# Kernel optimization log

Measured on AMD Instinct MI355X. Metric: run time of the kernel, lower is better.

## Reference

```python
import jax, jax.numpy as jnp
import numpy as np

EPS = 1e-8
SMOOTH = 9.0   # lambda_softmax
STEPS = 3      # iteration_step
SLOPE = 0.1    # LeakyReLU slope used by clipped_l2norm


def l2norm(x, axis=-1):
    # matches torch l2norm: x / (sqrt(sum x^2) + eps)
    return x / (jnp.sqrt(jnp.sum(x * x, axis=axis, keepdims=True)) + EPS)


def cos_sim(a, b, axis=-1):
    num = jnp.sum(a * b, axis=axis)
    den = jnp.linalg.norm(a, axis=axis) * jnp.linalg.norm(b, axis=axis)
    return num / jnp.maximum(den, EPS)


def duplicate_mask(cap):
    # same_word logic: cap_k identical to cap_c (off-diagonal). Computed via
    # pairwise squared distances (one GEMM) instead of O(B^2 L d) direct compare.
    B = cap.shape[0]
    flat = cap.reshape(B, -1)
    sq = jnp.sum(flat * flat, axis=1)
    d2 = sq[:, None] + sq[None, :] - 2.0 * (flat @ flat.T)
    return (d2 <= 1e-6) & (~jnp.eye(B, dtype=bool))


def gated(q, a, Wl, bl, Wg, bg):
    cat = jnp.concatenate([q, a], axis=-1)            # (..., 2d)
    lin = jnp.tanh(cat @ Wl.T + bl)
    gate = jax.nn.sigmoid(cat @ Wg.T + bg)
    return q * gate + lin * (1.0 - gate)


def imram_forward(img, cap, W_lt2i, b_lt2i, W_gt2i, b_gt2i,
                  W_li2t, b_li2t, W_gi2t, b_gi2t):
    B, R, D = img.shape
    L = cap.shape[1]
    dup = duplicate_mask(cap)                         # symmetric
    total = jnp.zeros((B, B), img.dtype)              # [caption, image] (training=True transpose)

    # ---- text-to-image: query = caption words, context = image regions ----
    cap_e = jnp.broadcast_to(cap[:, None], (B, B, L, D))   # (cap c, img i, L, D)
    q = cap_e
    for _ in range(STEPS):
        attn = jnp.einsum('ird,cild->cirl', img, q)          # (c,i,R,L)
        attn = l2norm(jax.nn.leaky_relu(attn, SLOPE), axis=-1)   # clipped_l2norm over queryL
        attn = jax.nn.softmax(SMOOTH * attn, axis=2)             # softmax over source regions r
        wc = jnp.einsum('cirl,ird->cild', attn, img)             # weightedContext (c,i,L,D)
        sim = jnp.mean(cos_sim(cap_e, wc, axis=-1), axis=-1)    # (c,i)
        total = total + jnp.where(dup, -1.0, sim)
        q = l2norm(gated(q, wc, W_lt2i, b_lt2i, W_gt2i, b_gt2i), axis=-1)

    # ---- image-to-text: query = image regions, context = caption words ----
    img_e = jnp.broadcast_to(img[None], (B, B, R, D))
    q = img_e
    for _ in range(STEPS):
        attn = jnp.einsum('cld,cird->cilr', cap, q)          # (c,i,L,R)
        attn = l2norm(jax.nn.leaky_relu(attn, SLOPE), axis=-1)   # over queryL (= R)
        attn = jax.nn.softmax(SMOOTH * attn, axis=2)             # over source words l
        wc = jnp.einsum('cilr,cld->cird', attn, cap)             # (c,i,R,D)
        sim = jnp.mean(cos_sim(img_e, wc, axis=-1), axis=-1)
        total = total + jnp.where(dup, -1.0, sim)
        q = l2norm(gated(q, wc, W_li2t, b_li2t, W_gi2t, b_gi2t), axis=-1)

    return total


def setup_inputs() -> dict:
    key = jax.random.key(0)
    ks = jax.random.split(key, 8)
    B, R, L, D = 32, 36, 40, 1024
    img_emb = jax.random.normal(ks[0], (B, R, D), dtype=jnp.float32)
    cap_emb = jax.random.normal(ks[1], (B, L, D), dtype=jnp.float32)
    cap_lens = jax.random.randint(ks[2], (B,), 5, L + 1)
    s = 0.02
    W_lt2i = s * jax.random.normal(ks[3], (D, 2 * D), dtype=jnp.float32)
    W_gt2i = s * jax.random.normal(ks[4], (D, 2 * D), dtype=jnp.float32)
    W_li2t = s * jax.random.normal(ks[5], (D, 2 * D), dtype=jnp.float32)
    W_gi2t = s * jax.random.normal(ks[6], (D, 2 * D), dtype=jnp.float32)
    z = jnp.zeros((D,), jnp.float32)
    return {
        'img_emb': img_emb, 'cap_emb': cap_emb,
        'W_lt2i': W_lt2i, 'b_lt2i': z, 'W_gt2i': W_gt2i, 'b_gt2i': z,
        'W_li2t': W_li2t, 'b_li2t': z, 'W_gi2t': W_gi2t, 'b_gi2t': z,
        'cap_lens': cap_lens,
    }


def reference(img_emb, cap_emb, W_lt2i, b_lt2i, W_gt2i, b_gt2i,
              W_li2t, b_li2t, W_gi2t, b_gi2t, cap_lens):
    # cap_lens is read but never used by the original forward (n_word unused)
    return imram_forward(img_emb, cap_emb, W_lt2i, b_lt2i, W_gt2i, b_gt2i,
                         W_li2t, b_li2t, W_gi2t, b_gi2t)
```

## Files before the change

### kernel.cpp

```cpp
#include <hip/hip_runtime.h>
#include <stdint.h>
#include <math.h>

typedef unsigned short u16;
typedef unsigned int u32;

#define EPSF 1e-8f
#define SMOOTHF 9.0f
#define SLOPEF 0.1f

__device__ __forceinline__ u16 f2bf(float f) {
  union { float f; u32 u; } v; v.f = f;
  u32 u = v.u;
  u32 r = (u + 0x7FFFu + ((u >> 16) & 1u)) >> 16;
  return (u16)r;
}
__device__ __forceinline__ float bf2f(u16 h) {
  union { u32 u; float f; } v; v.u = ((u32)h) << 16;
  return v.f;
}

__device__ __forceinline__ float wave_red_sum(float x) {
#pragma unroll
  for (int off = 32; off; off >>= 1) x += __shfl_xor(x, off, 64);
  return x;
}

__device__ __forceinline__ float block_red_sum(float x) {
  __shared__ float rs[4];
  x = wave_red_sum(x);
  const int lane = threadIdx.x & 63, wv = threadIdx.x >> 6;
  if (lane == 0) rs[wv] = x;
  __syncthreads();
  float r = rs[0] + rs[1] + rs[2] + rs[3];
  __syncthreads();
  return r;
}

__global__ __launch_bounds__(256) void rownorm_kernel(
    const float* __restrict__ cap, const float* __restrict__ img,
    float* __restrict__ capn, float* __restrict__ imgn) {
  const int row = blockIdx.x;
  const float* p; float* o;
  if (row < 1280) { p = cap + (size_t)row * 1024; o = capn + row; }
  else            { p = img + (size_t)(row - 1280) * 1024; o = imgn + (row - 1280); }
  float ss = 0.f;
  for (int d = threadIdx.x; d < 1024; d += 256) { float v = p[d]; ss += v * v; }
  float t = block_red_sum(ss);
  if (threadIdx.x == 0) *o = sqrtf(t);
}

__global__ __launch_bounds__(256) void dup_kernel(
    const float* __restrict__ cap, int* __restrict__ dup) {
  const int b = blockIdx.x;
  const int c = b >> 5, i = b & 31;
  float ss = 0.f;
  if (c != i) {
    const float* A = cap + (size_t)c * 40960;
    const float* B = cap + (size_t)i * 40960;
    for (int e = threadIdx.x; e < 40960; e += 256) { float d = A[e] - B[e]; ss += d * d; }
  }
  float t = block_red_sum(ss);
  if (threadIdx.x == 0) dup[b] = (c != i && t <= 1e-6f) ? 1 : 0;
}

__global__ __launch_bounds__(256) void wconv_kernel(
    const float* __restrict__ Wl, const float* __restrict__ Wg, u16* __restrict__ out) {
  const size_t idx = ((size_t)blockIdx.x * 256 + threadIdx.x) * 4;
  const int n = (int)(idx >> 11);
  const int k = (int)(idx & 2047);
  const float* src = (n & 1) ? &Wg[(size_t)(n >> 1) * 2048 + k] : &Wl[(size_t)(n >> 1) * 2048 + k];
  float4 v = *(const float4*)src;
  ushort4 o;
  o.x = f2bf(v.x); o.y = f2bf(v.y); o.z = f2bf(v.z); o.w = f2bf(v.w);
  *(ushort4*)&out[idx] = o;
}

__global__ __launch_bounds__(256) void bfpad_kernel(
    const float* __restrict__ src, u16* __restrict__ dst, int nrows) {
  const int b = blockIdx.x;
  const int blk = b / 48, r = b - blk * 48;
  u16* orow = dst + (size_t)b * 1024;
  const int tid = threadIdx.x;
  ushort4 o = {0, 0, 0, 0};
  if (r < nrows) {
    const float4 v = *(const float4*)&src[((size_t)blk * nrows + r) * 1024 + tid * 4];
    o.x = f2bf(v.x); o.y = f2bf(v.y); o.z = f2bf(v.z); o.w = f2bf(v.w);
  }
  *(ushort4*)&orow[tid * 4] = o;
}

__global__ __launch_bounds__(256) void ss_kernel(
    const float* __restrict__ src, float* __restrict__ out, int nrows) {
  const int s = blockIdx.x, b = blockIdx.y;
  float* orow = out + ((size_t)b * 48 + s) * 64;
  __shared__ float Ls[1024];
  const int tid = threadIdx.x;
  if (s < nrows)
    *(float4*)&Ls[tid * 4] = *(const float4*)&src[((size_t)b * nrows + s) * 1024 + tid * 4];
  __syncthreads();
  const int s2 = tid >> 2, koff = (tid & 3) * 256;
  float acc = 0.f;
  if (s < nrows && s2 < nrows) {
    const float* r2 = src + ((size_t)b * nrows + s2) * 1024 + koff;
    for (int k = 0; k < 256; k += 4) {
      float4 a = *(const float4*)&Ls[koff + k];
      float4 bb = *(const float4*)&r2[k];
      acc += a.x * bb.x + a.y * bb.y + a.z * bb.z + a.w * bb.w;
    }
  }
  acc += __shfl_xor(acc, 1, 64);
  acc += __shfl_xor(acc, 2, 64);
  if ((tid & 3) == 0) orow[s2] = acc;
}

typedef short bf16x8 __attribute__((ext_vector_type(8)));
typedef float f32x4 __attribute__((ext_vector_type(4)));

#define GLDS(gp, lp)                                                                   \
  __builtin_amdgcn_global_load_lds((const __attribute__((address_space(1))) void*)(gp), \
                                   (__attribute__((address_space(3))) void*)(lp), 16, 0, 0)

__global__ __launch_bounds__(256) void gemm_flex_kernel(
    const u16* __restrict__ A, const u16* __restrict__ B, u16* __restrict__ Cout,
    int koff, int trans) {
  __shared__ u16 As[128 * 32];
  __shared__ u16 Bs[128 * 32];
  const int tid = threadIdx.x;
  const int lane = tid & 63;
  const int wave = tid >> 6;
  const int wm = (wave >> 1) * 64;
  const int wn = (wave & 1) * 64;
  const int bm = blockIdx.x * 128;
  const int bn = blockIdx.y * 128;
  const int lr = lane & 15;
  const int lq = lane >> 4;
  f32x4 acc[4][4] = {};
  const int e0 = tid * 8;
  const int r0 = e0 >> 5;
  const int c0 = e0 & 31;
  const u16* Ag0 = A + (size_t)(bm + r0) * 1024 + c0;
  const u16* Ag1 = A + (size_t)(bm + r0 + 64) * 1024 + c0;
  const u16* Bg0 = B + (size_t)(bn + r0) * 2048 + koff + c0;
  const u16* Bg1 = B + (size_t)(bn + r0 + 64) * 2048 + koff + c0;
  u16* As0 = As + e0; u16* As1 = As + e0 + 2048;
  u16* Bs0 = Bs + e0; u16* Bs1 = Bs + e0 + 2048;
  for (int k0 = 0; k0 < 1024; k0 += 32) {
    GLDS(Ag0 + k0, As0);
    GLDS(Ag1 + k0, As1);
    GLDS(Bg0 + k0, Bs0);
    GLDS(Bg1 + k0, Bs1);
    __syncthreads();
    bf16x8 af[4], bfr[4];
#pragma unroll
    for (int mi = 0; mi < 4; mi++)
      af[mi] = *(const bf16x8*)&As[(wm + mi * 16 + lr) * 32 + lq * 8];
#pragma unroll
    for (int ni = 0; ni < 4; ni++)
      bfr[ni] = *(const bf16x8*)&Bs[(wn + ni * 16 + lr) * 32 + lq * 8];
#pragma unroll
    for (int mi = 0; mi < 4; mi++)
#pragma unroll
      for (int ni = 0; ni < 4; ni++)
        acc[mi][ni] = __builtin_amdgcn_mfma_f32_16x16x32_bf16(af[mi], bfr[ni], acc[mi][ni], 0, 0, 0);
    __syncthreads();
  }
#pragma unroll
  for (int mi = 0; mi < 4; mi++) {
#pragma unroll
    for (int ni = 0; ni < 4; ni++) {
      const int col = bn + wn + ni * 16 + lr;
      const int rowb = bm + wm + mi * 16 + lq * 4;
      if (!trans) {
#pragma unroll
        for (int r = 0; r < 4; r++)
          Cout[(size_t)(rowb + r) * 2048 + col] = f2bf(acc[mi][ni][r]);
      } else {
#pragma unroll
        for (int r = 0; r < 4; r++) {
          const int m = rowb + r;
          const int blk = m / 48, s = m - blk * 48;
          Cout[((size_t)blk * 2048 + col) * 64 + s] = f2bf(acc[mi][ni][r]);
        }
      }
    }
  }
}

__global__ __launch_bounds__(256) void gemm_e_kernel(
    const u16* __restrict__ A, const u16* __restrict__ B, float* __restrict__ C) {
  __shared__ u16 As[128 * 32];
  __shared__ u16 Bs[128 * 32];
  const int tid = threadIdx.x;
  const int lane = tid & 63;
  const int wave = tid >> 6;
  const int wm = (wave >> 1) * 64;
  const int wn = (wave & 1) * 64;
  const int bm = blockIdx.x * 128;
  const int bn = blockIdx.y * 128;
  const int lr = lane & 15;
  const int lq = lane >> 4;
  f32x4 acc[4][4] = {};
  const int e0 = tid * 8;
  const int r0 = e0 >> 5;
  const int c0 = e0 & 31;
  const u16* Ag0 = A + (size_t)(bm + r0) * 1024 + c0;
  const u16* Ag1 = A + (size_t)(bm + r0 + 64) * 1024 + c0;
  const u16* Bg0 = B + (size_t)(bn + r0) * 1024 + c0;
  const u16* Bg1 = B + (size_t)(bn + r0 + 64) * 1024 + c0;
  u16* As0 = As + e0; u16* As1 = As + e0 + 2048;
  u16* Bs0 = Bs + e0; u16* Bs1 = Bs + e0 + 2048;
  for (int k0 = 0; k0 < 1024; k0 += 32) {
    GLDS(Ag0 + k0, As0);
    GLDS(Ag1 + k0, As1);
    GLDS(Bg0 + k0, Bs0);
    GLDS(Bg1 + k0, Bs1);
    __syncthreads();
    bf16x8 af[4], bfr[4];
#pragma unroll
    for (int mi = 0; mi < 4; mi++)
      af[mi] = *(const bf16x8*)&As[(wm + mi * 16 + lr) * 32 + lq * 8];
#pragma unroll
    for (int ni = 0; ni < 4; ni++)
      bfr[ni] = *(const bf16x8*)&Bs[(wn + ni * 16 + lr) * 32 + lq * 8];
#pragma unroll
    for (int mi = 0; mi < 4; mi++)
#pragma unroll
      for (int ni = 0; ni < 4; ni++)
        acc[mi][ni] = __builtin_amdgcn_mfma_f32_16x16x32_bf16(af[mi], bfr[ni], acc[mi][ni], 0, 0, 0);
    __syncthreads();
  }
#pragma unroll
  for (int mi = 0; mi < 4; mi++)
#pragma unroll
    for (int ni = 0; ni < 4; ni++) {
      const int col = bn + wn + ni * 16 + lr;
      const int rowb = bm + wm + mi * 16 + lq * 4;
#pragma unroll
      for (int r = 0; r < 4; r++)
        C[(size_t)(rowb + r) * 1536 + col] = acc[mi][ni][r];
    }
}

template <int STEP, int NQ>
__global__ __launch_bounds__(512, 2) void wcgate_kernel(
    const u16* __restrict__ attnTg, const u16* __restrict__ q2nd,
    const u16* __restrict__ qref, const u16* __restrict__ SWT,
    const u16* __restrict__ Wcat, const u16* __restrict__ qw0,
    const float* __restrict__ bl, const float* __restrict__ bg,
    u16* __restrict__ Uout, int p0, int swz) {
  constexpr int NT = (STEP == 1) ? 17 : 1;
  constexpr int BM = 128;
  constexpr int BUF = BM * 64 + 256 * 64;
  __shared__ u16 sh[65536];
  const int tid = threadIdx.x;
  const int lane = tid & 63;
  const int wave = tid >> 6;
  const int wr = wave >> 2, wc = wave & 3;
  const int wm = wr * 64;
  const int wn = wc * 64;
  const int lr = lane & 15, lq = lane >> 4;
  const int b = blockIdx.y * 8 + blockIdx.x;
  int bmi, bni;
  if (swz) { bmi = (b & 7) + (b >> 6) * 8; bni = (b >> 3) & 7; }
  else     { bmi = blockIdx.y; bni = blockIdx.x; }
  const int bm = bmi * BM;
  const int bn = bni * 256;
  const int sIdx = (p0 + bm / NQ) >> 5;
  f32x4 acc[4][4] = {};

  auto stage = [&](int t, u16* buf) {
#pragma unroll
    for (int p = 0; p < 2; p++) {
      const int c = p * 512 + tid;
      const int row = c >> 3, sub = c & 7;
      const int sw = (sub ^ (row & 7)) << 3;
      const u16* src;
      if (STEP == 1 && t >= 1)
        src = q2nd + (size_t)(bm + row) * 1024 + (t - 1) * 64 + sw;
      else
        src = attnTg + (size_t)(bm + row) * 64 + sw;
      GLDS(src, buf + c * 8);
    }
#pragma unroll
    for (int p = 0; p < 4; p++) {
      const int c = p * 512 + tid;
      const int row = c >> 3, sub = c & 7;
      const int sw = (sub ^ (row & 7)) << 3;
      const u16* src;
      if (STEP == 1 && t >= 1)
        src = Wcat + (size_t)(bn + row) * 2048 + (t - 1) * 64 + sw;
      else
        src = SWT + ((size_t)sIdx * 2048 + bn + row) * 64 + sw;
      GLDS(src, buf + BM * 64 + c * 8);
    }
  };

  stage(0, sh);
  __syncthreads();
  for (int t = 0; t < NT; ++t) {
    u16* cur = (t & 1) ? sh + BUF : sh;
    u16* nxt = (t & 1) ? sh : sh + BUF;
    if (t + 1 < NT) stage(t + 1, nxt);
    const u16* A = cur;
    const u16* B = cur + BM * 64;
#pragma unroll
    for (int kk = 0; kk < 2; kk++) {
      bf16x8 bfv[4];
#pragma unroll
      for (int ni = 0; ni < 4; ni++) {
        const int rb = wn + ni * 16 + lr;
        bfv[ni] = *(const bf16x8*)&B[rb * 64 + ((kk * 32 + lq * 8) ^ ((rb & 7) << 3))];
      }
#pragma unroll
      for (int mi = 0; mi < 4; mi++) {
        const int ra = wm + mi * 16 + lr;
        const bf16x8 af = *(const bf16x8*)&A[ra * 64 + ((kk * 32 + lq * 8) ^ ((ra & 7) << 3))];
#pragma unroll
        for (int ni = 0; ni < 4; ni++)
          acc[mi][ni] = __builtin_amdgcn_mfma_f32_16x16x32_bf16(af, bfv[ni], acc[mi][ni], 0, 0, 0);
      }
    }
    __syncthreads();
  }

  u16* const qvS = sh;
  u16* const qw0S = sh + 16384;
  u16* const stash = sh + 49152;
#pragma unroll
  for (int p = 0; p < 4; p++) {
    const int c = p * 512 + tid;
    const int row = c >> 4, j = c & 15;
    const u16* src;
    if (STEP == 1) {
      src = qref + (size_t)(bm + row) * 1024 + (bn >> 1) + j * 8;
    } else {
      const int m = bm + row;
      const int pl = m / NQ;
      const int q = m - pl * NQ;
      const int gs = ((p0 + pl) & 31) * 48 + q;
      src = qref + (size_t)gs * 1024 + (bn >> 1) + j * 8;
    }
    GLDS(src, qvS + c * 8);
  }
  if constexpr (STEP == 0) {
#pragma unroll
    for (int p = 0; p < 8; p++) {
      const int c = p * 512 + tid;
      const int row = c >> 5, j = c & 31;
      const int m = bm + row;
      const int pl = m / NQ;
      const int q = m - pl * NQ;
      const int gs = ((p0 + pl) & 31) * 48 + q;
      GLDS(qw0 + (size_t)gs * 2048 + bn + j * 8, qw0S + c * 8);
    }
  }
  __syncthreads();

  const bool evn = (lane & 1) == 0;
#pragma unroll
  for (int ni = 0; ni < 4; ni++) {
    const int ncol = wn + ni * 16 + lr;
    const int dloc = ncol >> 1;
    const float blv = bl[(bn >> 1) + dloc];
    const float bgv = bg[(bn >> 1) + dloc];
#pragma unroll
    for (int mi = 0; mi < 4; mi++) {
#pragma unroll
      for (int r = 0; r < 4; r++) {
        const int rl = wm + mi * 16 + lq * 4 + r;
        const float v = acc[mi][ni][r];
        const float o = __shfl_xor(v, 1, 64);
        float lin2 = (evn ? v : o) + blv;
        float gt = (evn ? o : v) + bgv;
        if constexpr (STEP == 0) {
          const u32 pair = *(const u32*)&qw0S[rl * 256 + dloc * 2];
          lin2 += bf2f((u16)(pair & 0xffffu));
          gt += bf2f((u16)(pair >> 16));
        }
        const float qv = bf2f(qvS[rl * 128 + dloc]);
        lin2 = fminf(fmaxf(lin2, -30.f), 30.f);
        gt = fminf(fmaxf(gt, -30.f), 30.f);
        const float gg = 1.f / (1.f + __expf(-gt));
        const float e2 = __expf(-2.f * lin2);
        const float th = (1.f - e2) / (1.f + e2);
        const float u = qv * gg + th * (1.f - gg);
        if (evn) stash[rl * 128 + dloc] = f2bf(u);
      }
    }
  }
  __syncthreads();
#pragma unroll
  for (int p = 0; p < 4; p++) {
    const int c = p * 512 + tid;
    const int row = c >> 4, j = c & 15;
    *(bf16x8*)(Uout + (size_t)(bm + row) * 1024 + (bn >> 1) + j * 8) =
        *(const bf16x8*)&stash[row * 128 + j * 8];
  }
}

__global__ __launch_bounds__(256) void qnorm_kernel(u16* __restrict__ Q) {
  const int m = blockIdx.x * 4 + (threadIdx.x >> 6);
  const int lane = threadIdx.x & 63;
  u16* p = Q + (size_t)m * 1024;
  float v[16];
  float ss = 0.f;
#pragma unroll
  for (int t = 0; t < 4; t++) {
    ushort4 uv = *(const ushort4*)&p[t * 256 + lane * 4];
    float a = bf2f(uv.x), b = bf2f(uv.y), c = bf2f(uv.z), dd = bf2f(uv.w);
    v[t * 4 + 0] = a; v[t * 4 + 1] = b; v[t * 4 + 2] = c; v[t * 4 + 3] = dd;
    ss += a * a + b * b + c * c + dd * dd;
  }
  ss = wave_red_sum(ss);
  const float inv = 1.f / (sqrtf(ss) + EPSF);
#pragma unroll
  for (int t = 0; t < 4; t++) {
    ushort4 ov;
    ov.x = f2bf(v[t * 4 + 0] * inv); ov.y = f2bf(v[t * 4 + 1] * inv);
    ov.z = f2bf(v[t * 4 + 2] * inv); ov.w = f2bf(v[t * 4 + 3] * inv);
    *(ushort4*)&p[t * 256 + lane * 4] = ov;
  }
}

template <int NS, int NQ>
__global__ __launch_bounds__(256) void attn_step_kernel(
    const u16* __restrict__ Sbf, const float* __restrict__ E,
    const float* __restrict__ SS, const float* __restrict__ refn,
    const u16* __restrict__ qsrc, u16* __restrict__ attnTg,
    const int* __restrict__ dup, float* __restrict__ total,
    int p0, int t2i, int step) {
  constexpr int NQW = NQ / 4;
  const int pl = blockIdx.x;
  const int plg = p0 + pl;
  const int sIdx = plg >> 5, rIdx = plg & 31;
  const int c = t2i ? rIdx : sIdx;
  const int i = t2i ? sIdx : rIdx;
  const int gp = c * 32 + i;
  const u16* Sb = Sbf + (size_t)sIdx * 48 * 1024;
  const float* rn = refn + (size_t)rIdx * NQ;
  const u16* Qb = qsrc + (size_t)pl * NQ * 1024;

  __shared__ float redbuf[9600];
  __shared__ float attnS[2304];
  __shared__ float redcos[48];
  float* Elw = redbuf;
  float* SSl = redbuf + 3120;

  const int tid = threadIdx.x;
  const int lane = tid & 63, wave = tid >> 6;
  const int lr = lane & 15, quad = lane >> 4;

  if (step == 0) {
    for (int e = tid; e < 2304; e += 256) {
      int s, q; float v;
      if (t2i) { s = e / 48; q = e - s * 48; v = E[(size_t)(i * 48 + s) * 1536 + c * 48 + q]; }
      else     { q = e / 48; s = e - q * 48; v = E[(size_t)(i * 48 + q) * 1536 + c * 48 + s]; }
      attnS[s * 48 + q] = v;
    }
  } else {
    f32x4 acc[3][3] = {};
    const int kw = wave * 256;
    const u16* Arow[3]; const u16* Brow[3];
#pragma unroll
    for (int a = 0; a < 3; a++) {
      Arow[a] = Sb + (size_t)(a * 16 + lr) * 1024 + quad * 8;
      Brow[a] = Qb + (size_t)(a * 16 + lr) * 1024 + quad * 8;
    }
    bf16x8 A0[3], B0[3], A1[3], B1[3];
#pragma unroll
    for (int a = 0; a < 3; a++) {
      A0[a] = *(const bf16x8*)(Arow[a] + kw);
      B0[a] = *(const bf16x8*)(Brow[a] + kw);
    }
#pragma unroll
    for (int j = 0; j < 8; j++) {
      if (j < 7) {
        const int kn = kw + (j + 1) * 32;
#pragma unroll
        for (int a = 0; a < 3; a++) {
          A1[a] = *(const bf16x8*)(Arow[a] + kn);
          B1[a] = *(const bf16x8*)(Brow[a] + kn);
        }
      }
#pragma unroll
      for (int a = 0; a < 3; a++)
#pragma unroll
        for (int b = 0; b < 3; b++)
          acc[a][b] = __builtin_amdgcn_mfma_f32_16x16x32_bf16(A0[a], B0[b], acc[a][b], 0, 0, 0);
#pragma unroll
      for (int a = 0; a < 3; a++) { A0[a] = A1[a]; B0[a] = B1[a]; }
    }
    float* myred = redbuf + wave * 2400;
#pragma unroll
    for (int a = 0; a < 3; a++)
#pragma unroll
      for (int b = 0; b < 3; b++) {
        const int col = b * 16 + lr;
        const int row0 = a * 16 + quad * 4;
#pragma unroll
        for (int r = 0; r < 4; r++)
          myred[(row0 + r) * 50 + col] = acc[a][b][r];
      }
    __syncthreads();
#pragma unroll
    for (int t = 0; t < 9; t++) {
      const int e = tid + t * 256;
      const int s = e / 48, q = e - s * 48;
      const int o = s * 50 + q;
      attnS[e] = redbuf[o] + redbuf[2400 + o] + redbuf[4800 + o] + redbuf[7200 + o];
    }
  }
  __syncthreads();
  for (int e = tid; e < 2304; e += 256) {
    int s, q; float v;
    if (t2i) { s = e / 48; q = e - s * 48; v = E[(size_t)(i * 48 + s) * 1536 + c * 48 + q]; }
    else     { q = e / 48; s = e - q * 48; v = E[(size_t)(i * 48 + q) * 1536 + c * 48 + s]; }
    Elw[s * 65 + q] = v;
  }
  for (int e = tid; e < 48 * 64; e += 256) {
    const int s = e >> 6, s2 = e & 63;
    SSl[s * 65 + s2] = SS[((size_t)sIdx * 48 + s) * 64 + s2];
  }
  if (tid < NS) {
    float row[NQ];
    float ss = 0.f;
#pragma unroll
    for (int q = 0; q < NQ; q++) {
      float v = attnS[tid * 48 + q];
      v = (v > 0.f) ? v : SLOPEF * v;
      row[q] = v; ss += v * v;
    }
    const float inv = 1.f / (sqrtf(ss) + EPSF);
#pragma unroll
    for (int q = 0; q < NQ; q++) attnS[tid * 48 + q] = row[q] * inv;
  }
  __syncthreads();
  if (tid < NQ) {
    float mx = -1e30f;
#pragma unroll
    for (int s = 0; s < NS; s++) mx = fmaxf(mx, attnS[s * 48 + tid]);
    float ex[NS]; float sum = 0.f;
#pragma unroll
    for (int s = 0; s < NS; s++) {
      float t = __expf(SMOOTHF * (attnS[s * 48 + tid] - mx));
      ex[s] = t; sum += t;
    }
    const float inv = 1.f / sum;
#pragma unroll
    for (int s = 0; s < NS; s++) attnS[s * 48 + tid] = ex[s] * inv;
  }
  __syncthreads();
  if (step < 2) {
    for (int e = tid; e < NQ * 64; e += 256) {
      const int q = e >> 6, s = e & 63;
      attnTg[((size_t)(pl * NQ + q)) * 64 + s] = (s < 48) ? f2bf(attnS[s * 48 + q]) : (u16)0;
    }
  }
  {
    const int qbase = wave * NQW;
#pragma unroll
    for (int qq = 0; qq < NQW; qq++) {
      const int q = qbase + qq;
      const float a_l = (lane < 48) ? attnS[lane * 48 + q] : 0.f;
      float t = 0.f;
#pragma unroll
      for (int s = 0; s < NS; s++)
        t += attnS[s * 48 + q] * SSl[s * 65 + lane];
      float pssv = wave_red_sum(a_l * t);
      float numv = wave_red_sum(a_l * Elw[lane * 65 + q]);
      if (lane == 0) redcos[q] = numv / fmaxf(rn[q] * sqrtf(pssv), EPSF);
    }
  }
  __syncthreads();
  if (tid == 0) {
    float sim = 0.f;
#pragma unroll
    for (int q = 0; q < NQ; q++) sim += redcos[q];
    sim *= (1.0f / NQ);
    atomicAdd(&total[gp], dup[gp] ? -1.0f : sim);
  }
}

extern "C" void kernel_launch(void* const* d_in, const int* in_sizes, int n_in,
                              void* d_out, int out_size, void* d_ws, size_t ws_size,
                              hipStream_t stream) {
  (void)in_sizes; (void)n_in;
  const float* img = (const float*)d_in[0];
  const float* cap = (const float*)d_in[1];
  const float* W_lt2i = (const float*)d_in[2];
  const float* b_lt2i = (const float*)d_in[3];
  const float* W_gt2i = (const float*)d_in[4];
  const float* b_gt2i = (const float*)d_in[5];
  const float* W_li2t = (const float*)d_in[6];
  const float* b_li2t = (const float*)d_in[7];
  const float* W_gi2t = (const float*)d_in[8];
  const float* b_gi2t = (const float*)d_in[9];
  float* total = (float*)d_out;

  char* ws = (char*)d_ws;
  size_t off = 0;
  auto alloc = [&](size_t b) { void* p = ws + off; off += (b + 255) & ~(size_t)255; return p; };
  u16* Wcat = (u16*)alloc((size_t)2048 * 2048 * 2);
  u16* imgbf = (u16*)alloc((size_t)32 * 48 * 1024 * 2);
  u16* capbf = (u16*)alloc((size_t)32 * 48 * 1024 * 2);
  float* capn = (float*)alloc(1280 * 4);
  float* imgn = (float*)alloc(1152 * 4);
  int* dupb = (int*)alloc(1024 * 4);
  u16* SWT = (u16*)alloc((size_t)32 * 2048 * 64 * 2);
  float* E = (float*)alloc((size_t)1536 * 1536 * 4);
  float* SSi = (float*)alloc((size_t)32 * 48 * 64 * 4);
  float* SSc = (float*)alloc((size_t)32 * 48 * 64 * 4);
  u16* QW0 = (u16*)alloc((size_t)1536 * 2048 * 2);
  const size_t fixed = off;

  static const int cands[6] = {1024, 512, 256, 128, 64, 32};
  int P = 32;
  for (int ci = 0; ci < 6; ci++) {
    const int cand = cands[ci];
    const size_t cA = (((size_t)cand * 40 * 1024 * 2) + 255) & ~(size_t)255;
    const size_t aT = (((size_t)cand * 40 * 64 * 2) + 255) & ~(size_t)255;
    if (fixed + 2 * cA + aT <= ws_size) { P = cand; break; }
  }
  u16* catA = (u16*)alloc((size_t)P * 40 * 1024 * 2);
  u16* catB = (u16*)alloc((size_t)P * 40 * 1024 * 2);
  u16* attnTg = (u16*)alloc((size_t)P * 40 * 64 * 2);

  hipMemsetAsync(d_out, 0, (size_t)out_size * sizeof(float), stream);
  hipMemsetAsync(SWT, 0, (size_t)32 * 2048 * 64 * 2, stream);
  rownorm_kernel<<<dim3(2432), dim3(256), 0, stream>>>(cap, img, capn, imgn);
  dup_kernel<<<dim3(1024), dim3(256), 0, stream>>>(cap, dupb);
  bfpad_kernel<<<dim3(1536), dim3(256), 0, stream>>>(cap, capbf, 40);
  bfpad_kernel<<<dim3(1536), dim3(256), 0, stream>>>(img, imgbf, 36);
  gemm_e_kernel<<<dim3(12, 12), dim3(256), 0, stream>>>(imgbf, capbf, E);
  ss_kernel<<<dim3(48, 32), dim3(256), 0, stream>>>(img, SSi, 36);
  ss_kernel<<<dim3(48, 32), dim3(256), 0, stream>>>(cap, SSc, 40);

  const int nch = 1024 / P;
  for (int dir = 0; dir < 2; dir++) {
    const int t2i = (dir == 0) ? 1 : 0;
    const float* Wl = t2i ? W_lt2i : W_li2t;
    const float* Wg = t2i ? W_gt2i : W_gi2t;
    const float* bl = t2i ? b_lt2i : b_li2t;
    const float* bg = t2i ? b_gt2i : b_gi2t;
    const u16* Sbf = t2i ? imgbf : capbf;
    const u16* Refbf = t2i ? capbf : imgbf;
    const float* SSd = t2i ? SSi : SSc;
    const float* refn = t2i ? capn : imgn;
    const int NQ = t2i ? 40 : 36;
    const int Mrows = P * NQ;
    const int Mt = Mrows / 128;
    const int swz = (Mt % 8 == 0) ? 1 : 0;
    wconv_kernel<<<dim3(4096), dim3(256), 0, stream>>>(Wl, Wg, Wcat);
    gemm_flex_kernel<<<dim3(12, 16), dim3(256), 0, stream>>>(Sbf, Wcat, SWT, 1024, 1);
    gemm_flex_kernel<<<dim3(12, 16), dim3(256), 0, stream>>>(Refbf, Wcat, QW0, 0, 0);
    for (int ch = 0; ch < nch; ch++) {
      const int p0 = ch * P;
      for (int step = 0; step < 3; step++) {
        const u16* qsrc = (step == 1) ? catB : catA;
        if (t2i)
          attn_step_kernel<36, 40><<<dim3(P), dim3(256), 0, stream>>>(
              Sbf, E, SSd, refn, qsrc, attnTg, dupb, total, p0, 1, step);
        else
          attn_step_kernel<40, 36><<<dim3(P), dim3(256), 0, stream>>>(
              Sbf, E, SSd, refn, qsrc, attnTg, dupb, total, p0, 0, step);
        if (step == 0) {
          if (t2i)
            wcgate_kernel<0, 40><<<dim3(8, Mt), dim3(512), 0, stream>>>(
                attnTg, catA, Refbf, SWT, Wcat, QW0, bl, bg, catB, p0, swz);
          else
            wcgate_kernel<0, 36><<<dim3(8, Mt), dim3(512), 0, stream>>>(
                attnTg, catA, Refbf, SWT, Wcat, QW0, bl, bg, catB, p0, swz);
          qnorm_kernel<<<dim3(Mrows / 4), dim3(256), 0, stream>>>(catB);
        } else if (step == 1) {
          if (t2i)
            wcgate_kernel<1, 40><<<dim3(8, Mt), dim3(512), 0, stream>>>(
                attnTg, catB, catB, SWT, Wcat, QW0, bl, bg, catA, p0, swz);
          else
            wcgate_kernel<1, 36><<<dim3(8, Mt), dim3(512), 0, stream>>>(
                attnTg, catB, catB, SWT, Wcat, QW0, bl, bg, catA, p0, swz);
          qnorm_kernel<<<dim3(Mrows / 4), dim3(256), 0, stream>>>(catA);
        }
      }
    }
  }
}
```

Measured before the change: 1.656 ms.

## Overlap epilogue operand loads with GEMM main loop in wcgate kernel

Issues the epilogue's global-to-LDS loads (qref and qw0 tiles) during the final or only GEMM k-step rather than after the loop, using a partial vmcnt wait in the STEP 0 path. It also precomputes per-thread load addresses, fully unrolls the 17-step loop, and rebalances the gated epilogue so even and odd lanes each handle one row instead of idling half the lanes. It drops the occupancy hint of two blocks per CU and enlarges shared memory for STEP 0, which may reduce occupancy.

```diff
diff --git a/kernel.cpp b/kernel.cpp
--- a/kernel.cpp
+++ b/kernel.cpp
@@ -243,22 +243,20 @@
 }
 
 template <int STEP, int NQ>
-__global__ __launch_bounds__(512, 2) void wcgate_kernel(
+__global__ __launch_bounds__(512) void wcgate_kernel(
     const u16* __restrict__ attnTg, const u16* __restrict__ q2nd,
     const u16* __restrict__ qref, const u16* __restrict__ SWT,
     const u16* __restrict__ Wcat, const u16* __restrict__ qw0,
     const float* __restrict__ bl, const float* __restrict__ bg,
     u16* __restrict__ Uout, int p0, int swz) {
-  constexpr int NT = (STEP == 1) ? 17 : 1;
   constexpr int BM = 128;
-  constexpr int BUF = BM * 64 + 256 * 64;
-  __shared__ u16 sh[65536];
+  constexpr int BUF = 24576;
+  __shared__ u16 sh[(STEP == 0) ? 73728 : 65536];
   const int tid = threadIdx.x;
   const int lane = tid & 63;
   const int wave = tid >> 6;
   const int wr = wave >> 2, wc = wave & 3;
-  const int wm = wr * 64;
-  const int wn = wc * 64;
+  const int wm = wr * 64, wn = wc * 64;
   const int lr = lane & 15, lq = lane >> 4;
   const int b = blockIdx.y * 8 + blockIdx.x;
   int bmi, bni;
@@ -269,41 +267,63 @@
   const int sIdx = (p0 + bm / NQ) >> 5;
   f32x4 acc[4][4] = {};
 
-  auto stage = [&](int t, u16* buf) {
-#pragma unroll
-    for (int p = 0; p < 2; p++) {
-      const int c = p * 512 + tid;
-      const int row = c >> 3, sub = c & 7;
-      const int sw = (sub ^ (row & 7)) << 3;
-      const u16* src;
-      if (STEP == 1 && t >= 1)
-        src = q2nd + (size_t)(bm + row) * 1024 + (t - 1) * 64 + sw;
-      else
-        src = attnTg + (size_t)(bm + row) * 64 + sw;
-      GLDS(src, buf + c * 8);
-    }
+  int aoff[2]; const u16* asrc0[2]; const u16* asrcW[2];
+  int boff[4]; const u16* bsrc0[4]; const u16* bsrcW[4];
+#pragma unroll
+  for (int p = 0; p < 2; p++) {
+    const int c = p * 512 + tid;
+    const int row = c >> 3, sub = c & 7;
+    const int sw = (sub ^ (row & 7)) << 3;
+    aoff[p] = c * 8;
+    asrc0[p] = attnTg + (size_t)(bm + row) * 64 + sw;
+    asrcW[p] = q2nd + (size_t)(bm + row) * 1024 + sw;
+  }
+#pragma unroll
+  for (int p = 0; p < 4; p++) {
+    const int c = p * 512 + tid;
+    const int row = c >> 3, sub = c & 7;
+    const int sw = (sub ^ (row & 7)) << 3;
+    boff[p] = c * 8;
+    bsrc0[p] = SWT + ((size_t)sIdx * 2048 + bn + row) * 64 + sw;
+    bsrcW[p] = Wcat + (size_t)(bn + row) * 2048 + sw;
+  }
+
+  u16* const qvS = (STEP == 0) ? sh + 24576 : sh + 49152;
+  u16* const qw0S = sh + 40960;
+  u16* const stash = sh;
+
+  auto epi_stage = [&]() {
 #pragma unroll
     for (int p = 0; p < 4; p++) {
       const int c = p * 512 + tid;
-      const int row = c >> 3, sub = c & 7;
-      const int sw = (sub ^ (row & 7)) << 3;
+      const int row = c >> 4, j = c & 15;
       const u16* src;
-      if (STEP == 1 && t >= 1)
-        src = Wcat + (size_t)(bn + row) * 2048 + (t - 1) * 64 + sw;
-      else
-        src = SWT + ((size_t)sIdx * 2048 + bn + row) * 64 + sw;
-      GLDS(src, buf + BM * 64 + c * 8);
+      if (STEP == 1) {
+        src = qref + (size_t)(bm + row) * 1024 + (bn >> 1) + j * 8;
+      } else {
+        const int m = bm + row;
+        const int pl = m / NQ;
+        const int q = m - pl * NQ;
+        const int gs = ((p0 + pl) & 31) * 48 + q;
+        src = qref + (size_t)gs * 1024 + (bn >> 1) + j * 8;
+      }
+      GLDS(src, qvS + c * 8);
+    }
+    if (STEP == 0) {
+#pragma unroll
+      for (int p = 0; p < 8; p++) {
+        const int c = p * 512 + tid;
+        const int row = c >> 5, j = c & 31;
+        const int m = bm + row;
+        const int pl = m / NQ;
+        const int q = m - pl * NQ;
+        const int gs = ((p0 + pl) & 31) * 48 + q;
+        GLDS(qw0 + (size_t)gs * 2048 + bn + j * 8, qw0S + c * 8);
+      }
     }
   };
 
-  stage(0, sh);
-  __syncthreads();
-  for (int t = 0; t < NT; ++t) {
-    u16* cur = (t & 1) ? sh + BUF : sh;
-    u16* nxt = (t & 1) ? sh : sh + BUF;
-    if (t + 1 < NT) stage(t + 1, nxt);
-    const u16* A = cur;
-    const u16* B = cur + BM * 64;
+  auto compute = [&](const u16* A, const u16* B) {
 #pragma unroll
     for (int kk = 0; kk < 2; kk++) {
       bf16x8 bfv[4];
@@ -321,41 +341,41 @@
           acc[mi][ni] = __builtin_amdgcn_mfma_f32_16x16x32_bf16(af, bfv[ni], acc[mi][ni], 0, 0, 0);
       }
     }
+  };
+
+  if constexpr (STEP == 0) {
+#pragma unroll
+    for (int p = 0; p < 2; p++) GLDS(asrc0[p], sh + aoff[p]);
+#pragma unroll
+    for (int p = 0; p < 4; p++) GLDS(bsrc0[p], sh + 8192 + boff[p]);
+    epi_stage();
+    asm volatile("s_waitcnt vmcnt(12)" ::: "memory");
+    __builtin_amdgcn_sched_barrier(0);
+    __builtin_amdgcn_s_barrier();
+    compute(sh, sh + 8192);
     __syncthreads();
-  }
-
-  u16* const qvS = sh;
-  u16* const qw0S = sh + 16384;
-  u16* const stash = sh + 49152;
-#pragma unroll
-  for (int p = 0; p < 4; p++) {
-    const int c = p * 512 + tid;
-    const int row = c >> 4, j = c & 15;
-    const u16* src;
-    if (STEP == 1) {
-      src = qref + (size_t)(bm + row) * 1024 + (bn >> 1) + j * 8;
-    } else {
-      const int m = bm + row;
-      const int pl = m / NQ;
-      const int q = m - pl * NQ;
-      const int gs = ((p0 + pl) & 31) * 48 + q;
-      src = qref + (size_t)gs * 1024 + (bn >> 1) + j * 8;
-    }
-    GLDS(src, qvS + c * 8);
-  }
-  if constexpr (STEP == 0) {
-#pragma unroll
-    for (int p = 0; p < 8; p++) {
-      const int c = p * 512 + tid;
-      const int row = c >> 5, j = c & 31;
-      const int m = bm + row;
-      const int pl = m / NQ;
-      const int q = m - pl * NQ;
-      const int gs = ((p0 + pl) & 31) * 48 + q;
-      GLDS(qw0 + (size_t)gs * 2048 + bn + j * 8, qw0S + c * 8);
-    }
-  }
-  __syncthreads();
+  } else {
+#pragma unroll
+    for (int p = 0; p < 2; p++) GLDS(asrc0[p], sh + aoff[p]);
+#pragma unroll
+    for (int p = 0; p < 4; p++) GLDS(bsrc0[p], sh + 8192 + boff[p]);
+    __syncthreads();
+#pragma unroll
+    for (int tt = 0; tt < 17; ++tt) {
+      u16* cur = sh + (tt & 1) * BUF;
+      u16* nxt = sh + ((tt & 1) ^ 1) * BUF;
+      if (tt < 16) {
+#pragma unroll
+        for (int p = 0; p < 2; p++) GLDS(asrcW[p] + tt * 64, nxt + aoff[p]);
+#pragma unroll
+        for (int p = 0; p < 4; p++) GLDS(bsrcW[p] + tt * 64, nxt + 8192 + boff[p]);
+      } else {
+        epi_stage();
+      }
+      compute(cur, cur + 8192);
+      __syncthreads();
+    }
+  }
 
   const bool evn = (lane & 1) == 0;
 #pragma unroll
@@ -366,13 +386,16 @@
     const float bgv = bg[(bn >> 1) + dloc];
 #pragma unroll
     for (int mi = 0; mi < 4; mi++) {
-#pragma unroll
-      for (int r = 0; r < 4; r++) {
-        const int rl = wm + mi * 16 + lq * 4 + r;
-        const float v = acc[mi][ni][r];
-        const float o = __shfl_xor(v, 1, 64);
-        float lin2 = (evn ? v : o) + blv;
-        float gt = (evn ? o : v) + bgv;
+      const int base = wm + mi * 16 + lq * 4;
+#pragma unroll
+      for (int rr = 0; rr < 4; rr += 2) {
+        const float a0 = acc[mi][ni][rr];
+        const float a1 = acc[mi][ni][rr + 1];
+        const float o0 = __shfl_xor(a0, 1, 64);
+        const float o1 = __shfl_xor(a1, 1, 64);
+        float lin2 = (evn ? a0 : o1) + blv;
+        float gt = (evn ? o0 : a1) + bgv;
+        const int rl = base + rr + (evn ? 0 : 1);
         if constexpr (STEP == 0) {
           const u32 pair = *(const u32*)&qw0S[rl * 256 + dloc * 2];
           lin2 += bf2f((u16)(pair & 0xffffu));
@@ -385,7 +408,7 @@
         const float e2 = __expf(-2.f * lin2);
         const float th = (1.f - e2) / (1.f + e2);
         const float u = qv * gg + th * (1.f - gg);
-        if (evn) stash[rl * 128 + dloc] = f2bf(u);
+        stash[rl * 128 + dloc] = f2bf(u);
       }
     }
   }
```

Result: faster. 1.409 ms (-14.9%).
